# Kernel optimization log

Measured on AMD Instinct MI355X. Metric: run time of the kernel, lower is better.

The kernel has to match this reference:

```python
import jax, jax.numpy as jnp
import numpy as np

N_NODES = 50000
N_EDGES = 600000
N_RELS = 19
D_IN = 128
D_HID = 64
D_OUT = 2


def setup_inputs() -> dict:
    key = jax.random.key(0)
    ks = jax.random.split(key, 10)
    feat = jax.random.normal(ks[0], (N_NODES, D_IN), dtype=jnp.float32)
    src = jax.random.randint(ks[1], (N_EDGES,), 0, N_NODES)
    dst = jax.random.randint(ks[2], (N_EDGES,), 0, N_NODES)
    etype = jax.random.randint(ks[3], (N_EDGES,), 0, N_RELS)
    s1 = 1.0 / np.sqrt(D_IN)
    s2 = 1.0 / np.sqrt(D_HID)
    W1 = jax.random.normal(ks[4], (N_RELS, D_IN, D_HID), dtype=jnp.float32) * s1
    loop1 = jax.random.normal(ks[5], (D_IN, D_HID), dtype=jnp.float32) * s1
    b1 = jnp.zeros((D_HID,), dtype=jnp.float32)
    W2 = jax.random.normal(ks[6], (N_RELS, D_HID, D_OUT), dtype=jnp.float32) * s2
    loop2 = jax.random.normal(ks[7], (D_HID, D_OUT), dtype=jnp.float32) * s2
    b2 = jnp.zeros((D_OUT,), dtype=jnp.float32)
    return {"feat": feat, "W1": W1, "loop1": loop1, "b1": b1,
            "W2": W2, "loop2": loop2, "b2": b2,
            "src": src, "dst": dst, "etype": etype}


def _rel_graph_conv(h, W, loop_w, bias, src, dst, etype, activation):
    # Per-relation transform of all nodes: [N, R, O]; then gather per edge.
    # (num_rels * out_feat is small, so this is cheaper than gathering W per edge.)
    transformed = jnp.einsum('nd,rdo->nro', h, W)
    msg = transformed[src, etype]                      # [E, O] edge messages
    agg = jax.ops.segment_sum(msg, dst, num_segments=h.shape[0])  # scatter-add
    out = agg + h @ loop_w + bias                      # self-loop + bias
    if activation is not None:
        out = activation(out)
    return out


def reference(feat, W1, loop1, b1, W2, loop2, b2, src, dst, etype):
    h = _rel_graph_conv(feat, W1, loop1, b1, src, dst, etype, jax.nn.relu)
    h = _rel_graph_conv(h, W2, loop2, b2, src, dst, etype, None)
    return h
```

## Files before the change

kernel.cpp:

```cpp
#include <hip/hip_runtime.h>

#define N_NODES 50000
#define N_EDGES 600000
#define N_RELS  19
#define D_IN    128
#define D_HID   64
#define D_OUT   2
#define BSH     9
#define NB      ((N_NODES + 511) >> 9)
#define NSEG    (NB * N_RELS)
#define SL_BLOCKS  ((N_NODES + 63) / 64)
#define PREP_ELEMS (N_RELS * D_HID * D_IN + 48 * 64 + D_HID * D_IN)
#define PREP_BLOCKS ((PREP_ELEMS + 255) / 256)

typedef unsigned short u16;
typedef unsigned int   u32;
typedef __attribute__((ext_vector_type(8))) short sfrag;
typedef __attribute__((ext_vector_type(4))) float f32x4;

__device__ __forceinline__ u16 f2bf(float f){
  union { float f; u32 i; } v; v.f = f;
  u32 r = v.i + 0x7fffu + ((v.i >> 16) & 1u);
  return (u16)(r >> 16);
}
__device__ __forceinline__ float bf2f(u16 u){
  union { u32 i; float f; } v; v.i = ((u32)u) << 16; return v.f;
}
__device__ __forceinline__ u32 pack2(float lo, float hi){
  return (u32)f2bf(lo) | ((u32)f2bf(hi) << 16);
}

__global__ __launch_bounds__(256) void k_fused_pre(const float* __restrict__ feat,
                                                   u16* __restrict__ featb,
                                                   const int* __restrict__ src,
                                                   const int* __restrict__ et,
                                                   const int* __restrict__ dst,
                                                   int* __restrict__ seg_hist,
                                                   int* __restrict__ hist_dst){
  int i = blockIdx.x * 256 + threadIdx.x;
  float4 f = ((const float4*)feat)[i];
  uint2 p; p.x = pack2(f.x, f.y); p.y = pack2(f.z, f.w);
  ((uint2*)featb)[i] = p;
  if (i < N_EDGES) {
    int key = (src[i] >> BSH) * N_RELS + et[i];
    atomicAdd(&seg_hist[key * 16], 1);
    atomicAdd(&hist_dst[dst[i]], 1);
  }
}

__global__ __launch_bounds__(256) void k_alloc_scan(
    const int* __restrict__ hist_dst, int* __restrict__ dstart,
    int* __restrict__ cur_dst, int* __restrict__ gcnt,
    const int* __restrict__ seg_hist, int* __restrict__ seg_off,
    int* __restrict__ cur_seg,
    const float* __restrict__ W1, const float* __restrict__ loop1,
    const float* __restrict__ W2, u16* __restrict__ W1Tb,
    u16* __restrict__ loop1Tb, u16* __restrict__ W2allT){
  if (blockIdx.x >= 197) {
    int idx = (blockIdx.x - 197) * 256 + threadIdx.x;
    const int T1 = N_RELS * D_HID * D_IN;
    const int T2c = T1 + 48 * 64;
    const int T3 = T2c + D_HID * D_IN;
    if (idx < T1) {
      int r = idx / (D_HID * D_IN);
      int t = idx - r * (D_HID * D_IN);
      int j = t >> 7, d = t & 127;
      W1Tb[idx] = f2bf(W1[(r * D_IN + d) * D_HID + j]);
    } else if (idx < T2c) {
      int k2 = idx - T1;
      int n = k2 >> 6, k = k2 & 63;
      float val = 0.f;
      if (n < N_RELS * D_OUT) {
        int r = n >> 1, o = n & 1;
        val = W2[(r * D_HID + k) * D_OUT + o];
      }
      W2allT[k2] = f2bf(val);
    } else if (idx < T3) {
      int k2 = idx - T2c;
      int j = k2 >> 7, d = k2 & 127;
      loop1Tb[k2] = f2bf(loop1[d * D_HID + j]);
    }
    return;
  }
  if (blockIdx.x == 196) {
    __shared__ int se_s[256];
    int tid = threadIdx.x;
    const int PER = (NSEG + 255) / 256;
    int lo = tid * PER, hi = lo + PER; if (hi > NSEG) hi = NSEG; if (lo > NSEG) lo = NSEG;
    int se = 0;
    for (int i = lo; i < hi; ++i) se += seg_hist[i * 16];
    se_s[tid] = se;
    __syncthreads();
    if (tid == 0) {
      int a = 0;
      for (int j = 0; j < 256; ++j) { int x = se_s[j]; se_s[j] = a; a += x; }
    }
    __syncthreads();
    int eo = se_s[tid];
    for (int i = lo; i < hi; ++i) {
      int c = seg_hist[i * 16];
      seg_off[i] = eo; cur_seg[i * 16] = eo;
      eo += c;
    }
    if (hi == NSEG) seg_off[NSEG] = eo;
    return;
  }
  __shared__ int wbase[4];
  int tid = threadIdx.x, lane = tid & 63, wv = tid >> 6;
  int n = blockIdx.x * 256 + tid;
  int v = (n < N_NODES) ? hist_dst[n] : 0;
  int x = v;
  #pragma unroll
  for (int o = 1; o < 64; o <<= 1) { int u = __shfl_up(x, o); if (lane >= o) x += u; }
  if (lane == 63) wbase[wv] = atomicAdd(gcnt, x);
  __syncthreads();
  int start = wbase[wv] + x - v;
  if (n < N_NODES) { dstart[n] = start; cur_dst[n] = start; }
}

__global__ __launch_bounds__(256) void k_scatter(const int* __restrict__ src,
                                                 const int* __restrict__ et,
                                                 int* __restrict__ cur_seg,
                                                 int* __restrict__ perm){
  int e = blockIdx.x * 256 + threadIdx.x;
  if (e >= N_EDGES) return;
  int key = (src[e] >> BSH) * N_RELS + et[e];
  int p = atomicAdd(&cur_seg[key * 16], 1);
  perm[p] = e;
}

__device__ __forceinline__ void gather_tile(
    const u16* __restrict__ featb, const int* __restrict__ src,
    const int* __restrict__ dst, const int* __restrict__ perm,
    int* __restrict__ cur_dst, int* __restrict__ srel,
    int ts, int c, int t0, int rel, int tid, int w, int r16, int c4,
    sfrag (&aN)[2][4], int& nextPos){
  int vc = c - t0; if (vc > 128) vc = 128;
  #pragma unroll
  for (int mt = 0; mt < 2; ++mt) {
    int row = w * 32 + mt * 16 + r16;
    int rr = row < vc ? row : vc - 1;
    int s = src[perm[ts + t0 + rr]];
    const u16* ap = featb + (size_t)s * D_IN + c4 * 8;
    #pragma unroll
    for (int kk = 0; kk < 4; ++kk)
      aN[mt][kk] = *(const sfrag*)(ap + kk * 32);
  }
  nextPos = -1;
  if (tid < 128 && tid < vc) {
    int e = perm[ts + t0 + tid];
    nextPos = atomicAdd(&cur_dst[dst[e]], 1);
    srel[nextPos] = (src[e] << 5) | rel;
  }
}

__global__ __launch_bounds__(256, 4) void k_se1(
    const u16* __restrict__ featb, const u16* __restrict__ W1Tb,
    const u16* __restrict__ loop1Tb, const float* __restrict__ b1,
    const int* __restrict__ src, const int* __restrict__ dst,
    const int* __restrict__ perm, const int* __restrict__ seg_off,
    int* __restrict__ cur_dst, int* __restrict__ srel,
    u16* __restrict__ msgbuf, u16* __restrict__ agg1b){
  __shared__ __align__(16) u16 Bls[64][136];
  __shared__ __align__(16) u16 msg[128][72];
  __shared__ int posIds[128];
  int tid = threadIdx.x, lane = tid & 63, w = tid >> 6;
  int r16 = lane & 15, c4 = lane >> 4;

  if (blockIdx.x >= NSEG) {
    int base = (blockIdx.x - NSEG) * 64;
    { int j = tid >> 2, sg = tid & 3;
      const uint4* g = (const uint4*)(loop1Tb + j * 128) + sg * 4;
      uint4* d = (uint4*)&Bls[j][sg * 32];
      d[0] = g[0]; d[1] = g[1]; d[2] = g[2]; d[3] = g[3]; }
    int arow = base + w * 16 + r16; if (arow >= N_NODES) arow = N_NODES - 1;
    sfrag aF[4];
    #pragma unroll
    for (int kk = 0; kk < 4; ++kk)
      aF[kk] = *(const sfrag*)(featb + (size_t)arow * D_IN + kk * 32 + c4 * 8);
    __syncthreads();
    #pragma unroll
    for (int ct = 0; ct < 4; ++ct) {
      f32x4 acc = {0.f, 0.f, 0.f, 0.f};
      #pragma unroll
      for (int kk = 0; kk < 4; ++kk) {
        sfrag bF = *(const sfrag*)&Bls[ct * 16 + r16][kk * 32 + c4 * 8];
        acc = __builtin_amdgcn_mfma_f32_16x16x32_bf16(aF[kk], bF, acc, 0, 0, 0);
      }
      int col = ct * 16 + r16;
      float bias = b1[col];
      #pragma unroll
      for (int reg = 0; reg < 4; ++reg) {
        float v = acc[reg] + bias;
        float o = __shfl_xor(v, 1);
        if (!(lane & 1)) {
          int orow = w * 16 + c4 * 4 + reg;
          *(u32*)&msg[orow][col] = pack2(v, o);
        }
      }
    }
    __syncthreads();
    { int row = tid >> 2, q = tid & 3;
      int n = base + row;
      if (n < N_NODES) {
        uint4 a0 = ((const uint4*)&msg[row][0])[q * 2];
        uint4 a1 = ((const uint4*)&msg[row][0])[q * 2 + 1];
        uint4* d = (uint4*)(agg1b + (size_t)n * D_HID + q * 16);
        d[0] = a0; d[1] = a1;
      } }
    return;
  }

  const int q8 = NSEG >> 3, r8 = NSEG & 7;
  int xcd = blockIdx.x & 7, cidx = blockIdx.x >> 3;
  int seg = (xcd < r8 ? xcd * (q8 + 1) : r8 * (q8 + 1) + (xcd - r8) * q8) + cidx;
  int ts = seg_off[seg], c = seg_off[seg + 1] - ts;
  if (c == 0) return;
  int rel = seg - (seg / N_RELS) * N_RELS;

  {
    int j = tid >> 2, sg = tid & 3;
    const uint4* g = (const uint4*)(W1Tb + ((size_t)rel * 64 + j) * 128) + sg * 4;
    uint4* d = (uint4*)&Bls[j][sg * 32];
    d[0] = g[0]; d[1] = g[1]; d[2] = g[2]; d[3] = g[3];
  }

  sfrag aN[2][4]; int nextPos;
  gather_tile(featb, src, dst, perm, cur_dst, srel, ts, c, 0, rel,
              tid, w, r16, c4, aN, nextPos);
  __syncthreads();

  for (int t0 = 0; t0 < c; t0 += 128) {
    sfrag aC[2][4];
    #pragma unroll
    for (int mt = 0; mt < 2; ++mt)
      #pragma unroll
      for (int kk = 0; kk < 4; ++kk) aC[mt][kk] = aN[mt][kk];
    int curPos = nextPos;
    if (t0 + 128 < c)
      gather_tile(featb, src, dst, perm, cur_dst, srel, ts, c, t0 + 128, rel,
                  tid, w, r16, c4, aN, nextPos);
    #pragma unroll
    for (int ct = 0; ct < 4; ++ct) {
      sfrag bF[4];
      #pragma unroll
      for (int kk = 0; kk < 4; ++kk)
        bF[kk] = *(const sfrag*)&Bls[ct * 16 + r16][kk * 32 + c4 * 8];
      #pragma unroll
      for (int mt = 0; mt < 2; ++mt) {
        f32x4 acc = {0.f, 0.f, 0.f, 0.f};
        #pragma unroll
        for (int kk = 0; kk < 4; ++kk)
          acc = __builtin_amdgcn_mfma_f32_16x16x32_bf16(aC[mt][kk], bF[kk], acc, 0, 0, 0);
        #pragma unroll
        for (int reg = 0; reg < 4; ++reg) {
          float v = acc[reg];
          float o = __shfl_xor(v, 1);
          if (!(lane & 1)) {
            int orow = w * 32 + mt * 16 + c4 * 4 + reg;
            *(u32*)&msg[orow][ct * 16 + r16] = pack2(v, o);
          }
        }
      }
    }
    if (tid < 128) posIds[tid] = curPos;
    __syncthreads();
    { int row = tid >> 1, half = tid & 1;
      int pos = posIds[row];
      if (pos >= 0) {
        const uint4* mr = (const uint4*)&msg[row][half * 32];
        uint4* d = (uint4*)(msgbuf + (size_t)pos * D_HID + half * 32);
        d[0] = mr[0]; d[1] = mr[1]; d[2] = mr[2]; d[3] = mr[3];
      } }
    __syncthreads();
  }
}

__global__ __launch_bounds__(256) void k_agg_relu_self2(
    const u16* __restrict__ msgbuf, const int* __restrict__ dstart,
    const int* __restrict__ cnt, const u16* __restrict__ agg1b,
    const float* __restrict__ loop2, const float* __restrict__ b2,
    u16* __restrict__ h1b, float* __restrict__ out){
  int wv = threadIdx.x >> 6, lane = threadIdx.x & 63;
  int n = blockIdx.x * 4 + wv;
  int s = dstart[n], epos = s + cnt[n];
  int h = lane >> 5, c = lane & 31;
  float a0 = 0.f, a1 = 0.f;
  for (int i = s + h; i < epos; i += 2) {
    u32 v = ((const u32*)msgbuf)[(size_t)i * 32 + c];
    a0 += bf2f((u16)(v & 0xffffu));
    a1 += bf2f((u16)(v >> 16));
  }
  a0 += __shfl_down(a0, 32);
  a1 += __shfl_down(a1, 32);
  float p0 = 0.f, p1 = 0.f;
  if (h == 0) {
    u32 sv = ((const u32*)agg1b)[(size_t)n * 32 + c];
    float v0 = a0 + bf2f((u16)(sv & 0xffffu));
    float v1 = a1 + bf2f((u16)(sv >> 16));
    v0 = v0 > 0.f ? v0 : 0.f;
    v1 = v1 > 0.f ? v1 : 0.f;
    ((u32*)h1b)[(size_t)n * 32 + c] = (u32)f2bf(v0) | ((u32)f2bf(v1) << 16);
    float2 w0 = ((const float2*)loop2)[2 * c];
    float2 w1 = ((const float2*)loop2)[2 * c + 1];
    p0 = v0 * w0.x + v1 * w1.x;
    p1 = v0 * w0.y + v1 * w1.y;
  }
  #pragma unroll
  for (int off = 16; off; off >>= 1) {
    p0 += __shfl_down(p0, off);
    p1 += __shfl_down(p1, off);
  }
  if (lane == 0) {
    out[n * 2]     = p0 + b2[0];
    out[n * 2 + 1] = p1 + b2[1];
  }
}

__global__ __launch_bounds__(256) void k_t2(
    const u16* __restrict__ h1b, const u16* __restrict__ W2allT,
    float* __restrict__ T2){
  __shared__ __align__(16) u16 Bls[48][72];
  int tid = threadIdx.x, lane = tid & 63, w = tid >> 6;
  int r16 = lane & 15, c4 = lane >> 4;
  for (int idx = tid; idx < 48 * 8; idx += 256) {
    int row = idx >> 3, q = idx & 7;
    ((uint4*)&Bls[row][0])[q] = ((const uint4*)W2allT)[idx];
  }
  int base = blockIdx.x * 64;
  int arow = base + w * 16 + r16; if (arow >= N_NODES) arow = N_NODES - 1;
  sfrag aF[2];
  #pragma unroll
  for (int kk = 0; kk < 2; ++kk)
    aF[kk] = *(const sfrag*)(h1b + (size_t)arow * D_HID + kk * 32 + c4 * 8);
  __syncthreads();
  #pragma unroll
  for (int ct = 0; ct < 3; ++ct) {
    f32x4 acc = {0.f, 0.f, 0.f, 0.f};
    #pragma unroll
    for (int kk = 0; kk < 2; ++kk) {
      sfrag bF = *(const sfrag*)&Bls[ct * 16 + r16][kk * 32 + c4 * 8];
      acc = __builtin_amdgcn_mfma_f32_16x16x32_bf16(aF[kk], bF, acc, 0, 0, 0);
    }
    int col = ct * 16 + r16;
    if (col < N_RELS * D_OUT) {
      #pragma unroll
      for (int reg = 0; reg < 4; ++reg) {
        int orow = base + w * 16 + c4 * 4 + reg;
        if (orow < N_NODES) T2[(size_t)orow * 40 + col] = acc[reg];
      }
    }
  }
}

__global__ __launch_bounds__(256) void k_fin(
    const float* __restrict__ T2, const int* __restrict__ srel,
    const int* __restrict__ dstart, const int* __restrict__ cnt,
    float* __restrict__ out){
  int wv = threadIdx.x >> 6, lane = threadIdx.x & 63;
  int n = blockIdx.x * 4 + wv;
  int s = dstart[n], c = cnt[n];
  float ax = 0.f, ay = 0.f;
  for (int i = lane; i < c; i += 64) {
    int sr = srel[s + i];
    const float* p = T2 + (size_t)(sr >> 5) * 40 + (sr & 31) * 2;
    ax += p[0]; ay += p[1];
  }
  #pragma unroll
  for (int off = 32; off; off >>= 1) {
    ax += __shfl_down(ax, off);
    ay += __shfl_down(ay, off);
  }
  if (lane == 0) {
    out[n * 2]     += ax;
    out[n * 2 + 1] += ay;
  }
}

extern "C" void kernel_launch(void* const* d_in, const int* in_sizes, int n_in,
                              void* d_out, int out_size, void* d_ws, size_t ws_size,
                              hipStream_t stream){
  const float* feat  = (const float*)d_in[0];
  const float* W1    = (const float*)d_in[1];
  const float* loop1 = (const float*)d_in[2];
  const float* b1    = (const float*)d_in[3];
  const float* W2    = (const float*)d_in[4];
  const float* loop2 = (const float*)d_in[5];
  const float* b2    = (const float*)d_in[6];
  const int* src     = (const int*)d_in[7];
  const int* dst     = (const int*)d_in[8];
  const int* et      = (const int*)d_in[9];
  float* out = (float*)d_out;

  char* w = (char*)d_ws;
  u16*   W1Tb     = (u16*)(w);
  u16*   W2allT   = (u16*)(w + 311296);
  u16*   loop1Tb  = (u16*)(w + 317440);
  int*   seg_hist = (int*)(w + 333824);
  int*   gcnt     = (int*)(w + 452992);
  int*   hist_dst = (int*)(w + 453056);
  int*   seg_off  = (int*)(w + 653056);
  int*   cur_seg  = (int*)(w + 660544);
  int*   dstart   = (int*)(w + 779712);
  int*   cur_dst  = (int*)(w + 979712);
  int*   perm     = (int*)(w + 1179712);
  int*   srel     = (int*)(w + 3579712);
  u16*   featb    = (u16*)(w + 5979712);
  float* T2f      = (float*)(w + 5979712);
  u16*   agg1b    = (u16*)(w + 18779712);
  u16*   h1b      = (u16*)(w + 25179712);
  u16*   msgbuf   = (u16*)(w + 31579712);

  hipMemsetAsync(w + 333824, 0, 319232, stream);
  k_fused_pre     <<<6250, 256, 0, stream>>>(feat, featb, src, et, dst, seg_hist, hist_dst);
  k_alloc_scan    <<<197 + PREP_BLOCKS, 256, 0, stream>>>(
                      hist_dst, dstart, cur_dst, gcnt, seg_hist, seg_off, cur_seg,
                      W1, loop1, W2, W1Tb, loop1Tb, W2allT);
  k_scatter       <<<2344,  256, 0, stream>>>(src, et, cur_seg, perm);
  k_se1           <<<NSEG + SL_BLOCKS, 256, 0, stream>>>(
                      featb, W1Tb, loop1Tb, b1, src, dst, perm, seg_off,
                      cur_dst, srel, msgbuf, agg1b);
  k_agg_relu_self2<<<12500, 256, 0, stream>>>(msgbuf, dstart, hist_dst, agg1b,
                                              loop2, b2, h1b, out);
  k_t2            <<<SL_BLOCKS, 256, 0, stream>>>(h1b, W2allT, T2f);
  k_fin           <<<12500, 256, 0, stream>>>(T2f, srel, dstart, hist_dst, out);
}
```

Measured before the change: 302.4 us.

## Fuse layer-2 transform into aggregation kernel and drop LDS staging in se1

The k_t2 MFMA kernel is removed. Each node's ReLU'd hidden vector is now multiplied by W2 and loop2 (packed together into a 64x64 bf16 table) directly inside the aggregation kernel using shared memory. That drops the h1b round-trip through global memory and one launch. In k_se1, the W1 and loop1 tiles are read straight from global/L2 instead of being staged in LDS. The block-wide syncs and the software-pipelined gather are replaced by per-wave independent work with shuffles, and occupancy is raised to 6 blocks per SM. The risks are more redundant global reads of the weights, the loss of gather prefetch overlap, and a scalar 64-wide dot product per lane in k_agg.

```diff
diff --git a/kernel.cpp b/kernel.cpp
--- a/kernel.cpp
+++ b/kernel.cpp
@@ -9,8 +9,8 @@
 #define BSH     9
 #define NB      ((N_NODES + 511) >> 9)
 #define NSEG    (NB * N_RELS)
-#define SL_BLOCKS  ((N_NODES + 63) / 64)
-#define PREP_ELEMS (N_RELS * D_HID * D_IN + 48 * 64 + D_HID * D_IN)
+#define SL_BLOCKS ((N_NODES + 63) / 64)
+#define PREP_ELEMS (N_RELS * D_HID * D_IN + 64 * 64 + D_HID * D_IN)
 #define PREP_BLOCKS ((PREP_ELEMS + 255) / 256)
 
 typedef unsigned short u16;
@@ -30,13 +30,13 @@
   return (u32)f2bf(lo) | ((u32)f2bf(hi) << 16);
 }
 
-__global__ __launch_bounds__(256) void k_fused_pre(const float* __restrict__ feat,
-                                                   u16* __restrict__ featb,
-                                                   const int* __restrict__ src,
-                                                   const int* __restrict__ et,
-                                                   const int* __restrict__ dst,
-                                                   int* __restrict__ seg_hist,
-                                                   int* __restrict__ hist_dst){
+__global__ __launch_bounds__(256) void k_pre(const float* __restrict__ feat,
+                                             u16* __restrict__ featb,
+                                             const int* __restrict__ src,
+                                             const int* __restrict__ et,
+                                             const int* __restrict__ dst,
+                                             int* __restrict__ seg_hist,
+                                             int* __restrict__ hist_dst){
   int i = blockIdx.x * 256 + threadIdx.x;
   float4 f = ((const float4*)feat)[i];
   uint2 p; p.x = pack2(f.x, f.y); p.y = pack2(f.z, f.w);
@@ -48,19 +48,20 @@
   }
 }
 
-__global__ __launch_bounds__(256) void k_alloc_scan(
+__global__ __launch_bounds__(256) void k_prep(
     const int* __restrict__ hist_dst, int* __restrict__ dstart,
     int* __restrict__ cur_dst, int* __restrict__ gcnt,
     const int* __restrict__ seg_hist, int* __restrict__ seg_off,
     int* __restrict__ cur_seg,
     const float* __restrict__ W1, const float* __restrict__ loop1,
-    const float* __restrict__ W2, u16* __restrict__ W1Tb,
-    u16* __restrict__ loop1Tb, u16* __restrict__ W2allT){
+    const float* __restrict__ W2, const float* __restrict__ loop2,
+    u16* __restrict__ W1Tb, u16* __restrict__ loop1Tb,
+    u16* __restrict__ W2allT){
   if (blockIdx.x >= 197) {
     int idx = (blockIdx.x - 197) * 256 + threadIdx.x;
-    const int T1 = N_RELS * D_HID * D_IN;
-    const int T2c = T1 + 48 * 64;
-    const int T3 = T2c + D_HID * D_IN;
+    const int T1  = N_RELS * D_HID * D_IN;
+    const int T2c = T1 + 64 * 64;
+    const int T3  = T2c + D_HID * D_IN;
     if (idx < T1) {
       int r = idx / (D_HID * D_IN);
       int t = idx - r * (D_HID * D_IN);
@@ -68,12 +69,11 @@
       W1Tb[idx] = f2bf(W1[(r * D_IN + d) * D_HID + j]);
     } else if (idx < T2c) {
       int k2 = idx - T1;
-      int n = k2 >> 6, k = k2 & 63;
+      int j = k2 >> 6, k = k2 & 63;
       float val = 0.f;
-      if (n < N_RELS * D_OUT) {
-        int r = n >> 1, o = n & 1;
-        val = W2[(r * D_HID + k) * D_OUT + o];
-      }
+      if (j < N_RELS * D_OUT)      val = W2[((j >> 1) * D_HID + k) * D_OUT + (j & 1)];
+      else if (j == 38)            val = loop2[k * 2];
+      else if (j == 39)            val = loop2[k * 2 + 1];
       W2allT[k2] = f2bf(val);
     } else if (idx < T3) {
       int k2 = idx - T2c;
@@ -83,20 +83,17 @@
     return;
   }
   if (blockIdx.x == 196) {
-    __shared__ int se_s[256];
+    __shared__ int ps[256];
     int tid = threadIdx.x;
     const int PER = (NSEG + 255) / 256;
     int lo = tid * PER, hi = lo + PER; if (hi > NSEG) hi = NSEG; if (lo > NSEG) lo = NSEG;
-    int se = 0;
-    for (int i = lo; i < hi; ++i) se += seg_hist[i * 16];
-    se_s[tid] = se;
+    int s = 0;
+    for (int i = lo; i < hi; ++i) s += seg_hist[i * 16];
+    ps[tid] = s;
     __syncthreads();
-    if (tid == 0) {
-      int a = 0;
-      for (int j = 0; j < 256; ++j) { int x = se_s[j]; se_s[j] = a; a += x; }
-    }
+    if (tid == 0) { int a = 0; for (int j = 0; j < 256; ++j) { int x = ps[j]; ps[j] = a; a += x; } }
     __syncthreads();
-    int eo = se_s[tid];
+    int eo = ps[tid];
     for (int i = lo; i < hi; ++i) {
       int c = seg_hist[i * 16];
       seg_off[i] = eo; cur_seg[i * 16] = eo;
@@ -129,84 +126,47 @@
   perm[p] = e;
 }
 
-__device__ __forceinline__ void gather_tile(
-    const u16* __restrict__ featb, const int* __restrict__ src,
-    const int* __restrict__ dst, const int* __restrict__ perm,
-    int* __restrict__ cur_dst, int* __restrict__ srel,
-    int ts, int c, int t0, int rel, int tid, int w, int r16, int c4,
-    sfrag (&aN)[2][4], int& nextPos){
-  int vc = c - t0; if (vc > 128) vc = 128;
-  #pragma unroll
-  for (int mt = 0; mt < 2; ++mt) {
-    int row = w * 32 + mt * 16 + r16;
-    int rr = row < vc ? row : vc - 1;
-    int s = src[perm[ts + t0 + rr]];
-    const u16* ap = featb + (size_t)s * D_IN + c4 * 8;
-    #pragma unroll
-    for (int kk = 0; kk < 4; ++kk)
-      aN[mt][kk] = *(const sfrag*)(ap + kk * 32);
-  }
-  nextPos = -1;
-  if (tid < 128 && tid < vc) {
-    int e = perm[ts + t0 + tid];
-    nextPos = atomicAdd(&cur_dst[dst[e]], 1);
-    srel[nextPos] = (src[e] << 5) | rel;
-  }
-}
-
-__global__ __launch_bounds__(256, 4) void k_se1(
+__global__ __launch_bounds__(256, 6) void k_se1(
     const u16* __restrict__ featb, const u16* __restrict__ W1Tb,
     const u16* __restrict__ loop1Tb, const float* __restrict__ b1,
     const int* __restrict__ src, const int* __restrict__ dst,
     const int* __restrict__ perm, const int* __restrict__ seg_off,
     int* __restrict__ cur_dst, int* __restrict__ srel,
     u16* __restrict__ msgbuf, u16* __restrict__ agg1b){
-  __shared__ __align__(16) u16 Bls[64][136];
   __shared__ __align__(16) u16 msg[128][72];
-  __shared__ int posIds[128];
-  int tid = threadIdx.x, lane = tid & 63, w = tid >> 6;
+  int tid = threadIdx.x, lane = tid & 63, w4 = tid >> 6;
   int r16 = lane & 15, c4 = lane >> 4;
 
   if (blockIdx.x >= NSEG) {
     int base = (blockIdx.x - NSEG) * 64;
-    { int j = tid >> 2, sg = tid & 3;
-      const uint4* g = (const uint4*)(loop1Tb + j * 128) + sg * 4;
-      uint4* d = (uint4*)&Bls[j][sg * 32];
-      d[0] = g[0]; d[1] = g[1]; d[2] = g[2]; d[3] = g[3]; }
-    int arow = base + w * 16 + r16; if (arow >= N_NODES) arow = N_NODES - 1;
+    int arow = base + w4 * 16 + r16; if (arow >= N_NODES) arow = N_NODES - 1;
     sfrag aF[4];
     #pragma unroll
     for (int kk = 0; kk < 4; ++kk)
       aF[kk] = *(const sfrag*)(featb + (size_t)arow * D_IN + kk * 32 + c4 * 8);
-    __syncthreads();
-    #pragma unroll
     for (int ct = 0; ct < 4; ++ct) {
+      int col = ct * 16 + r16;
       f32x4 acc = {0.f, 0.f, 0.f, 0.f};
       #pragma unroll
       for (int kk = 0; kk < 4; ++kk) {
-        sfrag bF = *(const sfrag*)&Bls[ct * 16 + r16][kk * 32 + c4 * 8];
+        sfrag bF = *(const sfrag*)(loop1Tb + (size_t)col * D_IN + kk * 32 + c4 * 8);
         acc = __builtin_amdgcn_mfma_f32_16x16x32_bf16(aF[kk], bF, acc, 0, 0, 0);
       }
-      int col = ct * 16 + r16;
       float bias = b1[col];
       #pragma unroll
       for (int reg = 0; reg < 4; ++reg) {
         float v = acc[reg] + bias;
         float o = __shfl_xor(v, 1);
-        if (!(lane & 1)) {
-          int orow = w * 16 + c4 * 4 + reg;
-          *(u32*)&msg[orow][col] = pack2(v, o);
-        }
+        if (!(lane & 1))
+          *(u32*)&msg[w4 * 16 + c4 * 4 + reg][col] = pack2(v, o);
       }
     }
-    __syncthreads();
-    { int row = tid >> 2, q = tid & 3;
-      int n = base + row;
+    { int j = lane >> 2, q = lane & 3;
+      int n = base + w4 * 16 + j;
       if (n < N_NODES) {
-        uint4 a0 = ((const uint4*)&msg[row][0])[q * 2];
-        uint4 a1 = ((const uint4*)&msg[row][0])[q * 2 + 1];
+        const uint4* mr = (const uint4*)&msg[w4 * 16 + j][q * 16];
         uint4* d = (uint4*)(agg1b + (size_t)n * D_HID + q * 16);
-        d[0] = a0; d[1] = a1;
+        d[0] = mr[0]; d[1] = mr[1];
       } }
     return;
   }
@@ -217,144 +177,103 @@
   int ts = seg_off[seg], c = seg_off[seg + 1] - ts;
   if (c == 0) return;
   int rel = seg - (seg / N_RELS) * N_RELS;
-
-  {
-    int j = tid >> 2, sg = tid & 3;
-    const uint4* g = (const uint4*)(W1Tb + ((size_t)rel * 64 + j) * 128) + sg * 4;
-    uint4* d = (uint4*)&Bls[j][sg * 32];
-    d[0] = g[0]; d[1] = g[1]; d[2] = g[2]; d[3] = g[3];
-  }
-
-  sfrag aN[2][4]; int nextPos;
-  gather_tile(featb, src, dst, perm, cur_dst, srel, ts, c, 0, rel,
-              tid, w, r16, c4, aN, nextPos);
-  __syncthreads();
+  const u16* bp = W1Tb + (size_t)rel * (D_HID * D_IN);
 
   for (int t0 = 0; t0 < c; t0 += 128) {
-    sfrag aC[2][4];
+    int vc = c - t0; if (vc > 128) vc = 128;
+    int myPos = -1;
+    if (lane < 32) {
+      int row = w4 * 32 + lane;
+      if (row < vc) {
+        int e = perm[ts + t0 + row];
+        myPos = atomicAdd(&cur_dst[dst[e]], 1);
+        srel[myPos] = (src[e] << 5) | rel;
+      }
+    }
+    sfrag aF[2][4];
     #pragma unroll
-    for (int mt = 0; mt < 2; ++mt)
-      #pragma unroll
-      for (int kk = 0; kk < 4; ++kk) aC[mt][kk] = aN[mt][kk];
-    int curPos = nextPos;
-    if (t0 + 128 < c)
-      gather_tile(featb, src, dst, perm, cur_dst, srel, ts, c, t0 + 128, rel,
-                  tid, w, r16, c4, aN, nextPos);
-    #pragma unroll
+    for (int mt = 0; mt < 2; ++mt) {
+      int row = w4 * 32 + mt * 16 + r16;
+      int rr = row < vc ? row : vc - 1;
+      int s = src[perm[ts + t0 + rr]];
+      const u16* ap = featb + (size_t)s * D_IN + c4 * 8;
+      #pragma unroll
+      for (int kk = 0; kk < 4; ++kk)
+        aF[mt][kk] = *(const sfrag*)(ap + kk * 32);
+    }
     for (int ct = 0; ct < 4; ++ct) {
+      int col = ct * 16 + r16;
       sfrag bF[4];
       #pragma unroll
       for (int kk = 0; kk < 4; ++kk)
-        bF[kk] = *(const sfrag*)&Bls[ct * 16 + r16][kk * 32 + c4 * 8];
+        bF[kk] = *(const sfrag*)(bp + (size_t)col * D_IN + kk * 32 + c4 * 8);
       #pragma unroll
       for (int mt = 0; mt < 2; ++mt) {
         f32x4 acc = {0.f, 0.f, 0.f, 0.f};
         #pragma unroll
         for (int kk = 0; kk < 4; ++kk)
-          acc = __builtin_amdgcn_mfma_f32_16x16x32_bf16(aC[mt][kk], bF[kk], acc, 0, 0, 0);
+          acc = __builtin_amdgcn_mfma_f32_16x16x32_bf16(aF[mt][kk], bF[kk], acc, 0, 0, 0);
         #pragma unroll
         for (int reg = 0; reg < 4; ++reg) {
           float v = acc[reg];
           float o = __shfl_xor(v, 1);
-          if (!(lane & 1)) {
-            int orow = w * 32 + mt * 16 + c4 * 4 + reg;
-            *(u32*)&msg[orow][ct * 16 + r16] = pack2(v, o);
-          }
+          if (!(lane & 1))
+            *(u32*)&msg[w4 * 32 + mt * 16 + c4 * 4 + reg][col] = pack2(v, o);
         }
       }
     }
-    if (tid < 128) posIds[tid] = curPos;
-    __syncthreads();
-    { int row = tid >> 1, half = tid & 1;
-      int pos = posIds[row];
+    { int j = lane >> 1, half = lane & 1;
+      int pos = __shfl(myPos, j);
       if (pos >= 0) {
-        const uint4* mr = (const uint4*)&msg[row][half * 32];
+        const uint4* mr = (const uint4*)&msg[w4 * 32 + j][half * 32];
         uint4* d = (uint4*)(msgbuf + (size_t)pos * D_HID + half * 32);
         d[0] = mr[0]; d[1] = mr[1]; d[2] = mr[2]; d[3] = mr[3];
       } }
-    __syncthreads();
-  }
-}
-
-__global__ __launch_bounds__(256) void k_agg_relu_self2(
+  }
+}
+
+__global__ __launch_bounds__(256) void k_agg(
     const u16* __restrict__ msgbuf, const int* __restrict__ dstart,
     const int* __restrict__ cnt, const u16* __restrict__ agg1b,
-    const float* __restrict__ loop2, const float* __restrict__ b2,
-    u16* __restrict__ h1b, float* __restrict__ out){
-  int wv = threadIdx.x >> 6, lane = threadIdx.x & 63;
+    const u16* __restrict__ W2allT, const float* __restrict__ b2,
+    float* __restrict__ T2f, float* __restrict__ out){
+  __shared__ u16   W2ls[64][66];
+  __shared__ float h1s[4][68];
+  int tid = threadIdx.x, wv = tid >> 6, lane = tid & 63;
+  for (int i = tid; i < 64 * 64; i += 256) W2ls[i >> 6][i & 63] = W2allT[i];
   int n = blockIdx.x * 4 + wv;
   int s = dstart[n], epos = s + cnt[n];
-  int h = lane >> 5, c = lane & 31;
+  int h = lane >> 5, cc = lane & 31;
   float a0 = 0.f, a1 = 0.f;
   for (int i = s + h; i < epos; i += 2) {
-    u32 v = ((const u32*)msgbuf)[(size_t)i * 32 + c];
+    u32 v = ((const u32*)msgbuf)[(size_t)i * 32 + cc];
     a0 += bf2f((u16)(v & 0xffffu));
     a1 += bf2f((u16)(v >> 16));
   }
   a0 += __shfl_down(a0, 32);
   a1 += __shfl_down(a1, 32);
-  float p0 = 0.f, p1 = 0.f;
   if (h == 0) {
-    u32 sv = ((const u32*)agg1b)[(size_t)n * 32 + c];
+    u32 sv = ((const u32*)agg1b)[(size_t)n * 32 + cc];
     float v0 = a0 + bf2f((u16)(sv & 0xffffu));
     float v1 = a1 + bf2f((u16)(sv >> 16));
     v0 = v0 > 0.f ? v0 : 0.f;
     v1 = v1 > 0.f ? v1 : 0.f;
-    ((u32*)h1b)[(size_t)n * 32 + c] = (u32)f2bf(v0) | ((u32)f2bf(v1) << 16);
-    float2 w0 = ((const float2*)loop2)[2 * c];
-    float2 w1 = ((const float2*)loop2)[2 * c + 1];
-    p0 = v0 * w0.x + v1 * w1.x;
-    p1 = v0 * w0.y + v1 * w1.y;
-  }
-  #pragma unroll
-  for (int off = 16; off; off >>= 1) {
-    p0 += __shfl_down(p0, off);
-    p1 += __shfl_down(p1, off);
-  }
-  if (lane == 0) {
-    out[n * 2]     = p0 + b2[0];
-    out[n * 2 + 1] = p1 + b2[1];
-  }
-}
-
-__global__ __launch_bounds__(256) void k_t2(
-    const u16* __restrict__ h1b, const u16* __restrict__ W2allT,
-    float* __restrict__ T2){
-  __shared__ __align__(16) u16 Bls[48][72];
-  int tid = threadIdx.x, lane = tid & 63, w = tid >> 6;
-  int r16 = lane & 15, c4 = lane >> 4;
-  for (int idx = tid; idx < 48 * 8; idx += 256) {
-    int row = idx >> 3, q = idx & 7;
-    ((uint4*)&Bls[row][0])[q] = ((const uint4*)W2allT)[idx];
-  }
-  int base = blockIdx.x * 64;
-  int arow = base + w * 16 + r16; if (arow >= N_NODES) arow = N_NODES - 1;
-  sfrag aF[2];
-  #pragma unroll
-  for (int kk = 0; kk < 2; ++kk)
-    aF[kk] = *(const sfrag*)(h1b + (size_t)arow * D_HID + kk * 32 + c4 * 8);
+    h1s[wv][2 * cc]     = v0;
+    h1s[wv][2 * cc + 1] = v1;
+  }
   __syncthreads();
-  #pragma unroll
-  for (int ct = 0; ct < 3; ++ct) {
-    f32x4 acc = {0.f, 0.f, 0.f, 0.f};
-    #pragma unroll
-    for (int kk = 0; kk < 2; ++kk) {
-      sfrag bF = *(const sfrag*)&Bls[ct * 16 + r16][kk * 32 + c4 * 8];
-      acc = __builtin_amdgcn_mfma_f32_16x16x32_bf16(aF[kk], bF, acc, 0, 0, 0);
-    }
-    int col = ct * 16 + r16;
-    if (col < N_RELS * D_OUT) {
-      #pragma unroll
-      for (int reg = 0; reg < 4; ++reg) {
-        int orow = base + w * 16 + c4 * 4 + reg;
-        if (orow < N_NODES) T2[(size_t)orow * 40 + col] = acc[reg];
-      }
-    }
+  if (lane < 40) {
+    float acc = 0.f;
+    #pragma unroll 8
+    for (int k = 0; k < 64; ++k)
+      acc += bf2f(W2ls[lane][k]) * h1s[wv][k];
+    if (lane < 38) T2f[(size_t)n * 40 + lane] = acc;
+    else           out[n * 2 + (lane - 38)] = acc + b2[lane - 38];
   }
 }
 
 __global__ __launch_bounds__(256) void k_fin(
-    const float* __restrict__ T2, const int* __restrict__ srel,
+    const float* __restrict__ T2f, const int* __restrict__ srel,
     const int* __restrict__ dstart, const int* __restrict__ cnt,
     float* __restrict__ out){
   int wv = threadIdx.x >> 6, lane = threadIdx.x & 63;
@@ -363,7 +282,7 @@
   float ax = 0.f, ay = 0.f;
   for (int i = lane; i < c; i += 64) {
     int sr = srel[s + i];
-    const float* p = T2 + (size_t)(sr >> 5) * 40 + (sr & 31) * 2;
+    const float* p = T2f + (size_t)(sr >> 5) * 40 + (sr & 31) * 2;
     ax += p[0]; ay += p[1];
   }
   #pragma unroll
@@ -395,33 +314,31 @@
   char* w = (char*)d_ws;
   u16*   W1Tb     = (u16*)(w);
   u16*   W2allT   = (u16*)(w + 311296);
-  u16*   loop1Tb  = (u16*)(w + 317440);
-  int*   seg_hist = (int*)(w + 333824);
-  int*   gcnt     = (int*)(w + 452992);
-  int*   hist_dst = (int*)(w + 453056);
-  int*   seg_off  = (int*)(w + 653056);
-  int*   cur_seg  = (int*)(w + 660544);
-  int*   dstart   = (int*)(w + 779712);
-  int*   cur_dst  = (int*)(w + 979712);
-  int*   perm     = (int*)(w + 1179712);
-  int*   srel     = (int*)(w + 3579712);
-  u16*   featb    = (u16*)(w + 5979712);
-  float* T2f      = (float*)(w + 5979712);
-  u16*   agg1b    = (u16*)(w + 18779712);
-  u16*   h1b      = (u16*)(w + 25179712);
-  u16*   msgbuf   = (u16*)(w + 31579712);
-
-  hipMemsetAsync(w + 333824, 0, 319232, stream);
-  k_fused_pre     <<<6250, 256, 0, stream>>>(feat, featb, src, et, dst, seg_hist, hist_dst);
-  k_alloc_scan    <<<197 + PREP_BLOCKS, 256, 0, stream>>>(
-                      hist_dst, dstart, cur_dst, gcnt, seg_hist, seg_off, cur_seg,
-                      W1, loop1, W2, W1Tb, loop1Tb, W2allT);
-  k_scatter       <<<2344,  256, 0, stream>>>(src, et, cur_seg, perm);
-  k_se1           <<<NSEG + SL_BLOCKS, 256, 0, stream>>>(
-                      featb, W1Tb, loop1Tb, b1, src, dst, perm, seg_off,
-                      cur_dst, srel, msgbuf, agg1b);
-  k_agg_relu_self2<<<12500, 256, 0, stream>>>(msgbuf, dstart, hist_dst, agg1b,
-                                              loop2, b2, h1b, out);
-  k_t2            <<<SL_BLOCKS, 256, 0, stream>>>(h1b, W2allT, T2f);
-  k_fin           <<<12500, 256, 0, stream>>>(T2f, srel, dstart, hist_dst, out);
-}
+  u16*   loop1Tb  = (u16*)(w + 319488);
+  int*   seg_hist = (int*)(w + 335872);
+  int*   gcnt     = (int*)(w + 455040);
+  int*   hist_dst = (int*)(w + 455104);
+  int*   seg_off  = (int*)(w + 655104);
+  int*   cur_seg  = (int*)(w + 662592);
+  int*   dstart   = (int*)(w + 781760);
+  int*   cur_dst  = (int*)(w + 981760);
+  int*   perm     = (int*)(w + 1181760);
+  int*   srel     = (int*)(w + 3581760);
+  u16*   featb    = (u16*)(w + 5981760);
+  float* T2f      = (float*)(w + 5981760);
+  u16*   agg1b    = (u16*)(w + 18781760);
+  u16*   msgbuf   = (u16*)(w + 25181760);
+
+  hipMemsetAsync(w + 335872, 0, 319232, stream);
+  k_pre     <<<6250, 256, 0, stream>>>(feat, featb, src, et, dst, seg_hist, hist_dst);
+  k_prep    <<<197 + PREP_BLOCKS, 256, 0, stream>>>(
+                hist_dst, dstart, cur_dst, gcnt, seg_hist, seg_off, cur_seg,
+                W1, loop1, W2, loop2, W1Tb, loop1Tb, W2allT);
+  k_scatter <<<2344, 256, 0, stream>>>(src, et, cur_seg, perm);
+  k_se1     <<<NSEG + SL_BLOCKS, 256, 0, stream>>>(
+                featb, W1Tb, loop1Tb, b1, src, dst, perm, seg_off,
+                cur_dst, srel, msgbuf, agg1b);
+  k_agg     <<<12500, 256, 0, stream>>>(msgbuf, dstart, hist_dst, agg1b,
+                                        W2allT, b2, T2f, out);
+  k_fin     <<<12500, 256, 0, stream>>>(T2f, srel, dstart, hist_dst, out);
+}
```

After: 386.1 us. +27.7%, slower.
